# Performance work log

Hardware: AMD Instinct MI355X
Metric: run time of the kernel (lower is better)

## Reference

```python
import jax, jax.numpy as jnp
import numpy as np
import math
from jax import lax


def _conv1d(x, w, stride=1):
    """Cross-correlation (torch F.conv1d semantics), VALID. x:[B,L], w:[K] -> [B,Lout]."""
    out = lax.conv_general_dilated(
        x[:, None, :], w[None, None, :], window_strides=(stride,), padding='VALID',
        dimension_numbers=('NCH', 'OIH', 'NCH'))
    return out[:, 0, :]


def setup_inputs() -> dict:
    B, D, K, NS = 32768, 1024, 8, 10  # batch, dim, filter_length, num_sparse_params
    key = jax.random.key(0)
    k_x, k_lo, k_hi, k_sp = jax.random.split(key, 4)
    x = jax.random.normal(k_x, (B, D), dtype=jnp.float32)
    sqrt2 = math.sqrt(2.0)
    base_lo = jnp.array([1.0, 1.0], dtype=jnp.float32) / sqrt2
    base_hi = jnp.array([1.0, -1.0], dtype=jnp.float32) / sqrt2
    dec_lo = jnp.pad(base_lo, (0, K - 2)) + 0.01 * jax.random.normal(k_lo, (K,), jnp.float32)
    dec_hi = jnp.pad(base_hi, (0, K - 2)) + 0.01 * jax.random.normal(k_hi, (K,), jnp.float32)
    rec_lo = dec_lo  # cloned from dec at init
    rec_hi = dec_hi
    std = math.sqrt(2.0 / D)
    sparse_coeffs = std * jax.random.normal(k_sp, (NS,), jnp.float32)
    # distinct indices from randperm(dim), all < 2*coeff_len so all valid
    sparse_indices = jnp.asarray(np.random.default_rng(0).permutation(D)[:NS], dtype=jnp.int32)
    return {"x": x, "dec_lo": dec_lo, "dec_hi": dec_hi, "rec_lo": rec_lo,
            "rec_hi": rec_hi, "sparse_coeffs": sparse_coeffs,
            "sparse_indices": sparse_indices}


def reference(x, dec_lo, dec_hi, rec_lo, rec_hi, sparse_coeffs, sparse_indices):
    B, D = x.shape
    K = dec_lo.shape[0]
    p = K - 1  # reflect pad size = 7
    # ---- DWT: reflect pad, correlate with flipped dec filters, stride-2 downsample ----
    xp = jnp.pad(x, ((0, 0), (p, p)), mode='reflect')          # [B, D+14]
    lo = _conv1d(xp, dec_lo[::-1], stride=2)                   # [B, 516]
    hi = _conv1d(xp, dec_hi[::-1], stride=2)                   # [B, 516]
    Lc = lo.shape[1]
    # ---- sparse coefficient injection at fixed indices (distinct indices) ----
    flat = jnp.concatenate([lo, hi], axis=1)                   # [B, 2*Lc]
    flat = flat.at[:, sparse_indices].add(sparse_coeffs[None, :])
    lo2, hi2 = flat[:, :Lc], flat[:, Lc:2 * Lc]
    # ---- IDWT: zero-upsample, reflect pad, correlate with rec filters ----
    up_lo = jnp.zeros((B, 2 * Lc), x.dtype).at[:, ::2].set(lo2)
    up_hi = jnp.zeros((B, 2 * Lc), x.dtype).at[:, ::2].set(hi2)
    up_lo = jnp.pad(up_lo, ((0, 0), (p, p)), mode='reflect')
    up_hi = jnp.pad(up_hi, ((0, 0), (p, p)), mode='reflect')
    rec = _conv1d(up_lo, rec_lo) + _conv1d(up_hi, rec_hi)      # [B, 2*Lc + p] = [B, 1039]
    rec = rec[:, :D]                                           # crop to target length (1039 > 1024)
    return x + rec
```

## Files before the change

kernel.cpp:

```cpp
#include <hip/hip_runtime.h>

#define D_LEN 1024
#define K_LEN 8
#define NS    10
#define LCC   516
#define GRID  2048

__global__ __launch_bounds__(256) void wave_delta(
    const float* __restrict__ rec_lo, const float* __restrict__ rec_hi,
    const float* __restrict__ sp_c,   const int* __restrict__ sp_i,
    float* __restrict__ delta)
{
    __shared__ __align__(16) float2 st[512];
    const int tid = threadIdx.x;

    float frl[K_LEN], frh[K_LEN];
#pragma unroll
    for (int k = 0; k < K_LEN; ++k) { frl[k] = rec_lo[k]; frh[k] = rec_hi[k]; }

    float4 z; z.x = 0.f; z.y = 0.f; z.z = 0.f; z.w = 0.f;
    ((float4*)st)[tid] = z;
    __syncthreads();
    if (tid < NS) {
        const int s = sp_i[tid];
        const float v = sp_c[tid];
        if (s < 512)       st[s].x = v;
        else if (s >= LCC) st[s - LCC].y = v;
    }
    __syncthreads();

    float res0, res1, res2, res3;
    if (tid >= 2) {
        const float4 qa = ((const float4*)st)[tid - 2];
        const float4 qb = ((const float4*)st)[tid - 1];
        const float4 qc = ((const float4*)st)[tid];
        const float p0l = qa.z, p0h = qa.w;
        const float p1l = qb.x, p1h = qb.y;
        const float p2l = qb.z, p2h = qb.w;
        const float p3l = qc.x, p3h = qc.y;
        const float p4l = qc.z, p4h = qc.w;
        res0 = p0l*frl[1] + p0h*frh[1] + p1l*frl[3] + p1h*frh[3]
             + p2l*frl[5] + p2h*frh[5] + p3l*frl[7] + p3h*frh[7];
        res1 = p0l*frl[0] + p0h*frh[0] + p1l*frl[2] + p1h*frh[2]
             + p2l*frl[4] + p2h*frh[4] + p3l*frl[6] + p3h*frh[6];
        res2 = p1l*frl[1] + p1h*frh[1] + p2l*frl[3] + p2h*frh[3]
             + p3l*frl[5] + p3h*frh[5] + p4l*frl[7] + p4h*frh[7];
        res3 = p1l*frl[0] + p1h*frh[0] + p2l*frl[2] + p2h*frh[2]
             + p3l*frl[4] + p3h*frh[4] + p4l*frl[6] + p4h*frh[6];
    } else {
        float acc[4];
#pragma unroll
        for (int j = 0; j < 4; ++j) {
            const int t  = 4 * tid + j;
            const int k0 = ((j & 1) ^ 1);
            float a = 0.f;
#pragma unroll
            for (int i = 0; i < 4; ++i) {
                const int k = k0 + 2 * i;
                int m = t + k - 7;
                m = (m < 0) ? -m : m;
                const float2 pv = st[m >> 1];
                a = fmaf(pv.x, frl[k], a);
                a = fmaf(pv.y, frh[k], a);
            }
            acc[j] = a;
        }
        res0 = acc[0]; res1 = acc[1]; res2 = acc[2]; res3 = acc[3];
    }
    float4 r; r.x = res0; r.y = res1; r.z = res2; r.w = res3;
    ((float4*)delta)[tid] = r;
}

__global__ __launch_bounds__(256) void wavecore_kernel(
    const float* __restrict__ x,
    const float* __restrict__ dec_lo, const float* __restrict__ dec_hi,
    const float* __restrict__ rec_lo, const float* __restrict__ rec_hi,
    const float* __restrict__ delta,
    float* __restrict__ out, int J)
{
    __shared__ __align__(16) float  sx[2][D_LEN];
    __shared__ __align__(16) float2 st[512];

    const int tid = threadIdx.x;

    float fdl[K_LEN], fdh[K_LEN], frl[K_LEN], frh[K_LEN];
#pragma unroll
    for (int k = 0; k < K_LEN; ++k) {
        fdl[k] = dec_lo[k]; fdh[k] = dec_hi[k];
        frl[k] = rec_lo[k]; frh[k] = rec_hi[k];
    }
    const float4 dq = ((const float4*)delta)[tid];

    size_t off = (size_t)blockIdx.x * D_LEN + 4 * (size_t)tid;
    const size_t rstride = (size_t)GRID * D_LEN;
    float4 xv = *(const float4*)(x + off);
    ((float4*)sx[0])[tid] = xv;
    float4 xn;
    { xn = *(const float4*)(x + off + rstride); }
    __syncthreads();

    int cur = 0;
#pragma unroll 1
    for (int j = 0; j < J; ++j) {
        float4 xn2;
        if (j + 2 < J) xn2 = *(const float4*)(x + off + 2 * rstride);

        const float* sxc = sx[cur];
        float lo0 = 0.f, hi0 = 0.f, lo1 = 0.f, hi1 = 0.f;
        if (tid >= 2) {
            const float4 wa = ((const float4*)sxc)[tid - 2];
            const float4 wb = ((const float4*)sxc)[tid - 1];
            const float w[12] = { wa.x, wa.y, wa.z, wa.w,
                                  wb.x, wb.y, wb.z, wb.w,
                                  xv.x, xv.y, xv.z, xv.w };
#pragma unroll
            for (int jj = 0; jj < K_LEN; ++jj) {
                const float v0 = w[8  - jj];
                const float v1 = w[10 - jj];
                lo0 = fmaf(v0, fdl[jj], lo0);
                hi0 = fmaf(v0, fdh[jj], hi0);
                lo1 = fmaf(v1, fdl[jj], lo1);
                hi1 = fmaf(v1, fdh[jj], hi1);
            }
        } else {
#pragma unroll
            for (int q = 0; q < 2; ++q) {
                const int c = 2 * tid + q;
                float aL = 0.f, aH = 0.f;
#pragma unroll
                for (int jj = 0; jj < K_LEN; ++jj) {
                    int m = 2 * c - jj;
                    m = (m < 0) ? -m : m;
                    const float v = sxc[m];
                    aL = fmaf(v, fdl[jj], aL);
                    aH = fmaf(v, fdh[jj], aH);
                }
                if (q == 0) { lo0 = aL; hi0 = aH; }
                else        { lo1 = aL; hi1 = aH; }
            }
        }
        {
            float4 pr; pr.x = lo0; pr.y = hi0; pr.z = lo1; pr.w = hi1;
            ((float4*)st)[tid] = pr;
        }
        if (j + 1 < J) ((float4*)sx[cur ^ 1])[tid] = xn;
        __syncthreads();

        float res0, res1, res2, res3;
        if (tid >= 2) {
            const float4 qa = ((const float4*)st)[tid - 2];
            const float4 qb = ((const float4*)st)[tid - 1];
            const float p0l = qa.z, p0h = qa.w;
            const float p1l = qb.x, p1h = qb.y;
            const float p2l = qb.z, p2h = qb.w;
            const float p3l = lo0,  p3h = hi0;
            const float p4l = lo1,  p4h = hi1;
            res0 = p0l*frl[1] + p0h*frh[1] + p1l*frl[3] + p1h*frh[3]
                 + p2l*frl[5] + p2h*frh[5] + p3l*frl[7] + p3h*frh[7];
            res1 = p0l*frl[0] + p0h*frh[0] + p1l*frl[2] + p1h*frh[2]
                 + p2l*frl[4] + p2h*frh[4] + p3l*frl[6] + p3h*frh[6];
            res2 = p1l*frl[1] + p1h*frh[1] + p2l*frl[3] + p2h*frh[3]
                 + p3l*frl[5] + p3h*frh[5] + p4l*frl[7] + p4h*frh[7];
            res3 = p1l*frl[0] + p1h*frh[0] + p2l*frl[2] + p2h*frh[2]
                 + p3l*frl[4] + p3h*frh[4] + p4l*frl[6] + p4h*frh[6];
        } else {
            float acc[4];
#pragma unroll
            for (int jj = 0; jj < 4; ++jj) {
                const int t  = 4 * tid + jj;
                const int k0 = ((jj & 1) ^ 1);
                float a = 0.f;
#pragma unroll
                for (int i = 0; i < 4; ++i) {
                    const int k = k0 + 2 * i;
                    int m = t + k - 7;
                    m = (m < 0) ? -m : m;
                    const float2 pv = st[m >> 1];
                    a = fmaf(pv.x, frl[k], a);
                    a = fmaf(pv.y, frh[k], a);
                }
                acc[jj] = a;
            }
            res0 = acc[0]; res1 = acc[1]; res2 = acc[2]; res3 = acc[3];
        }

        float4 r;
        r.x = res0 + xv.x + dq.x;
        r.y = res1 + xv.y + dq.y;
        r.z = res2 + xv.z + dq.z;
        r.w = res3 + xv.w + dq.w;
        *(float4*)(out + off) = r;
        __syncthreads();

        xv = xn; xn = xn2; cur ^= 1; off += rstride;
    }
}

extern "C" void kernel_launch(void* const* d_in, const int* in_sizes, int n_in,
                              void* d_out, int out_size, void* d_ws, size_t ws_size,
                              hipStream_t stream) {
    const float* x      = (const float*)d_in[0];
    const float* dec_lo = (const float*)d_in[1];
    const float* dec_hi = (const float*)d_in[2];
    const float* rec_lo = (const float*)d_in[3];
    const float* rec_hi = (const float*)d_in[4];
    const float* sp_c   = (const float*)d_in[5];
    const int*   sp_i   = (const int*)d_in[6];
    float* out   = (float*)d_out;
    float* delta = (float*)d_ws;

    const int Brows = in_sizes[0] / D_LEN;
    const int J     = Brows / GRID;

    wave_delta<<<1, 256, 0, stream>>>(rec_lo, rec_hi, sp_c, sp_i, delta);
    wavecore_kernel<<<GRID, 256, 0, stream>>>(x, dec_lo, dec_hi, rec_lo, rec_hi,
                                              delta, out, J);
}
```

Baseline: 49.48 us.

## Fuse sparse delta computation into main kernel and double-buffer stage scratch

The separate single-block kernel that computed the sparse-coefficient reconstruction delta is removed. Every block of the main kernel now computes that delta itself in a short prologue. The shared subband buffer is double-buffered, so the trailing barrier in each row iteration can be dropped. This removes one kernel launch, its dependency gap and one barrier per row, at the cost of redundant per-block prologue work and more shared memory.

```diff
diff --git a/kernel.cpp b/kernel.cpp
--- a/kernel.cpp
+++ b/kernel.cpp
@@ -6,80 +6,15 @@
 #define LCC   516
 #define GRID  2048
 
-__global__ __launch_bounds__(256) void wave_delta(
-    const float* __restrict__ rec_lo, const float* __restrict__ rec_hi,
-    const float* __restrict__ sp_c,   const int* __restrict__ sp_i,
-    float* __restrict__ delta)
-{
-    __shared__ __align__(16) float2 st[512];
-    const int tid = threadIdx.x;
-
-    float frl[K_LEN], frh[K_LEN];
-#pragma unroll
-    for (int k = 0; k < K_LEN; ++k) { frl[k] = rec_lo[k]; frh[k] = rec_hi[k]; }
-
-    float4 z; z.x = 0.f; z.y = 0.f; z.z = 0.f; z.w = 0.f;
-    ((float4*)st)[tid] = z;
-    __syncthreads();
-    if (tid < NS) {
-        const int s = sp_i[tid];
-        const float v = sp_c[tid];
-        if (s < 512)       st[s].x = v;
-        else if (s >= LCC) st[s - LCC].y = v;
-    }
-    __syncthreads();
-
-    float res0, res1, res2, res3;
-    if (tid >= 2) {
-        const float4 qa = ((const float4*)st)[tid - 2];
-        const float4 qb = ((const float4*)st)[tid - 1];
-        const float4 qc = ((const float4*)st)[tid];
-        const float p0l = qa.z, p0h = qa.w;
-        const float p1l = qb.x, p1h = qb.y;
-        const float p2l = qb.z, p2h = qb.w;
-        const float p3l = qc.x, p3h = qc.y;
-        const float p4l = qc.z, p4h = qc.w;
-        res0 = p0l*frl[1] + p0h*frh[1] + p1l*frl[3] + p1h*frh[3]
-             + p2l*frl[5] + p2h*frh[5] + p3l*frl[7] + p3h*frh[7];
-        res1 = p0l*frl[0] + p0h*frh[0] + p1l*frl[2] + p1h*frh[2]
-             + p2l*frl[4] + p2h*frh[4] + p3l*frl[6] + p3h*frh[6];
-        res2 = p1l*frl[1] + p1h*frh[1] + p2l*frl[3] + p2h*frh[3]
-             + p3l*frl[5] + p3h*frh[5] + p4l*frl[7] + p4h*frh[7];
-        res3 = p1l*frl[0] + p1h*frh[0] + p2l*frl[2] + p2h*frh[2]
-             + p3l*frl[4] + p3h*frh[4] + p4l*frl[6] + p4h*frh[6];
-    } else {
-        float acc[4];
-#pragma unroll
-        for (int j = 0; j < 4; ++j) {
-            const int t  = 4 * tid + j;
-            const int k0 = ((j & 1) ^ 1);
-            float a = 0.f;
-#pragma unroll
-            for (int i = 0; i < 4; ++i) {
-                const int k = k0 + 2 * i;
-                int m = t + k - 7;
-                m = (m < 0) ? -m : m;
-                const float2 pv = st[m >> 1];
-                a = fmaf(pv.x, frl[k], a);
-                a = fmaf(pv.y, frh[k], a);
-            }
-            acc[j] = a;
-        }
-        res0 = acc[0]; res1 = acc[1]; res2 = acc[2]; res3 = acc[3];
-    }
-    float4 r; r.x = res0; r.y = res1; r.z = res2; r.w = res3;
-    ((float4*)delta)[tid] = r;
-}
-
 __global__ __launch_bounds__(256) void wavecore_kernel(
     const float* __restrict__ x,
     const float* __restrict__ dec_lo, const float* __restrict__ dec_hi,
     const float* __restrict__ rec_lo, const float* __restrict__ rec_hi,
-    const float* __restrict__ delta,
+    const float* __restrict__ sp_c,   const int* __restrict__ sp_i,
     float* __restrict__ out, int J)
 {
     __shared__ __align__(16) float  sx[2][D_LEN];
-    __shared__ __align__(16) float2 st[512];
+    __shared__ __align__(16) float2 st[2][512];
 
     const int tid = threadIdx.x;
 
@@ -89,17 +24,67 @@
         fdl[k] = dec_lo[k]; fdh[k] = dec_hi[k];
         frl[k] = rec_lo[k]; frh[k] = rec_hi[k];
     }
-    const float4 dq = ((const float4*)delta)[tid];
+
+    float dq0, dq1, dq2, dq3;
+    {
+        float4 z; z.x = 0.f; z.y = 0.f; z.z = 0.f; z.w = 0.f;
+        ((float4*)st[0])[tid] = z;
+        __syncthreads();
+        if (tid < NS) {
+            const int   s = sp_i[tid];
+            const float v = sp_c[tid];
+            if (s < 512)       st[0][s].x = v;
+            else if (s >= LCC) st[0][s - LCC].y = v;
+        }
+        __syncthreads();
+        if (tid >= 2) {
+            const float4 qa = ((const float4*)st[0])[tid - 2];
+            const float4 qb = ((const float4*)st[0])[tid - 1];
+            const float4 qc = ((const float4*)st[0])[tid];
+            const float p0l = qa.z, p0h = qa.w;
+            const float p1l = qb.x, p1h = qb.y;
+            const float p2l = qb.z, p2h = qb.w;
+            const float p3l = qc.x, p3h = qc.y;
+            const float p4l = qc.z, p4h = qc.w;
+            dq0 = p0l*frl[1] + p0h*frh[1] + p1l*frl[3] + p1h*frh[3]
+                + p2l*frl[5] + p2h*frh[5] + p3l*frl[7] + p3h*frh[7];
+            dq1 = p0l*frl[0] + p0h*frh[0] + p1l*frl[2] + p1h*frh[2]
+                + p2l*frl[4] + p2h*frh[4] + p3l*frl[6] + p3h*frh[6];
+            dq2 = p1l*frl[1] + p1h*frh[1] + p2l*frl[3] + p2h*frh[3]
+                + p3l*frl[5] + p3h*frh[5] + p4l*frl[7] + p4h*frh[7];
+            dq3 = p1l*frl[0] + p1h*frh[0] + p2l*frl[2] + p2h*frh[2]
+                + p3l*frl[4] + p3h*frh[4] + p4l*frl[6] + p4h*frh[6];
+        } else {
+            float acc[4];
+#pragma unroll
+            for (int j = 0; j < 4; ++j) {
+                const int t  = 4 * tid + j;
+                const int k0 = ((j & 1) ^ 1);
+                float a = 0.f;
+#pragma unroll
+                for (int i = 0; i < 4; ++i) {
+                    const int k = k0 + 2 * i;
+                    int m = t + k - 7;
+                    m = (m < 0) ? -m : m;
+                    const float2 pv = st[0][m >> 1];
+                    a = fmaf(pv.x, frl[k], a);
+                    a = fmaf(pv.y, frh[k], a);
+                }
+                acc[j] = a;
+            }
+            dq0 = acc[0]; dq1 = acc[1]; dq2 = acc[2]; dq3 = acc[3];
+        }
+        __syncthreads();
+    }
 
     size_t off = (size_t)blockIdx.x * D_LEN + 4 * (size_t)tid;
     const size_t rstride = (size_t)GRID * D_LEN;
     float4 xv = *(const float4*)(x + off);
     ((float4*)sx[0])[tid] = xv;
-    float4 xn;
-    { xn = *(const float4*)(x + off + rstride); }
+    float4 xn = *(const float4*)(x + off + rstride);
     __syncthreads();
 
-    int cur = 0;
+    int cur = 0, sb = 0;
 #pragma unroll 1
     for (int j = 0; j < J; ++j) {
         float4 xn2;
@@ -141,15 +126,15 @@
         }
         {
             float4 pr; pr.x = lo0; pr.y = hi0; pr.z = lo1; pr.w = hi1;
-            ((float4*)st)[tid] = pr;
+            ((float4*)st[sb])[tid] = pr;
         }
         if (j + 1 < J) ((float4*)sx[cur ^ 1])[tid] = xn;
         __syncthreads();
 
         float res0, res1, res2, res3;
         if (tid >= 2) {
-            const float4 qa = ((const float4*)st)[tid - 2];
-            const float4 qb = ((const float4*)st)[tid - 1];
+            const float4 qa = ((const float4*)st[sb])[tid - 2];
+            const float4 qb = ((const float4*)st[sb])[tid - 1];
             const float p0l = qa.z, p0h = qa.w;
             const float p1l = qb.x, p1h = qb.y;
             const float p2l = qb.z, p2h = qb.w;
@@ -175,7 +160,7 @@
                     const int k = k0 + 2 * i;
                     int m = t + k - 7;
                     m = (m < 0) ? -m : m;
-                    const float2 pv = st[m >> 1];
+                    const float2 pv = st[sb][m >> 1];
                     a = fmaf(pv.x, frl[k], a);
                     a = fmaf(pv.y, frh[k], a);
                 }
@@ -185,14 +170,13 @@
         }
 
         float4 r;
-        r.x = res0 + xv.x + dq.x;
-        r.y = res1 + xv.y + dq.y;
-        r.z = res2 + xv.z + dq.z;
-        r.w = res3 + xv.w + dq.w;
+        r.x = res0 + xv.x + dq0;
+        r.y = res1 + xv.y + dq1;
+        r.z = res2 + xv.z + dq2;
+        r.w = res3 + xv.w + dq3;
         *(float4*)(out + off) = r;
-        __syncthreads();
-
-        xv = xn; xn = xn2; cur ^= 1; off += rstride;
+
+        xv = xn; xn = xn2; cur ^= 1; sb ^= 1; off += rstride;
     }
 }
 
@@ -206,13 +190,11 @@
     const float* rec_hi = (const float*)d_in[4];
     const float* sp_c   = (const float*)d_in[5];
     const int*   sp_i   = (const int*)d_in[6];
-    float* out   = (float*)d_out;
-    float* delta = (float*)d_ws;
+    float* out = (float*)d_out;
 
     const int Brows = in_sizes[0] / D_LEN;
     const int J     = Brows / GRID;
 
-    wave_delta<<<1, 256, 0, stream>>>(rec_lo, rec_hi, sp_c, sp_i, delta);
     wavecore_kernel<<<GRID, 256, 0, stream>>>(x, dec_lo, dec_hi, rec_lo, rec_hi,
-                                              delta, out, J);
+                                              sp_c, sp_i, out, J);
 }
```

Result: faster. 46.62 us (-5.8%).
